# Performance work log

Hardware: AMD Instinct MI355X
Metric: run time of the kernel (lower is better)

## Reference

```python
import jax, jax.numpy as jnp
import numpy as np

NX = 96
N_NODES = 6 * NX * NX          # 55296 cubed-sphere grid points
N_EDGES = 4 * N_NODES          # ~4-neighbor connectivity
HID = 32
NUM_STEPS = 3


def setup_inputs() -> dict:
    key = jax.random.key(0)
    ks = jax.random.split(key, 12)
    s = 0.05
    inp = {
        "in_node_features": jax.random.normal(ks[0], (2, 6, NX, NX, 32), jnp.float32),
        "edge_relation": jax.random.normal(ks[1], (N_EDGES, 4), jnp.float32),
        "pw1": jax.random.normal(ks[2], (32, HID), jnp.float32) * s,
        "pb1": jnp.zeros((HID,), jnp.float32),
        "pw2": jax.random.normal(ks[3], (HID, HID), jnp.float32) * s,
        "pb2": jnp.zeros((HID,), jnp.float32),
        "ew1": jax.random.normal(ks[4], (4, 32), jnp.float32) * s,
        "eb1": jnp.zeros((32,), jnp.float32),
        "ew2": jax.random.normal(ks[5], (32, HID * HID), jnp.float32) * s,
        "eb2": jnp.zeros((HID * HID,), jnp.float32),
        "conv_b": jnp.zeros((HID,), jnp.float32),
        "gru_w_ih": jax.random.normal(ks[6], (3 * HID, HID), jnp.float32) * s,
        "gru_w_hh": jax.random.normal(ks[7], (3 * HID, HID), jnp.float32) * s,
        "gru_b_ih": jnp.zeros((3 * HID,), jnp.float32),
        "gru_b_hh": jnp.zeros((3 * HID,), jnp.float32),
        "edge_src": jax.random.randint(ks[8], (N_EDGES,), 0, N_NODES, jnp.int32),
        "edge_dst": jax.random.randint(ks[9], (N_EDGES,), 0, N_NODES, jnp.int32),
    }
    return inp


def reference(in_node_features, edge_relation, pw1, pb1, pw2, pb2,
              ew1, eb1, ew2, eb2, conv_b,
              gru_w_ih, gru_w_hh, gru_b_ih, gru_b_hh,
              edge_src, edge_dst):
    B, T, nx1, nx2, C = in_node_features.shape
    N = T * nx1 * nx2
    H = pw2.shape[1]

    x = in_node_features.reshape(B, N, C)
    # project_node_features: Linear -> ReLU -> Linear
    h0 = jnp.maximum(x @ pw1 + pb1, 0.0) @ pw2 + pb2          # [B, N, H]

    # edge network (same every step): Linear -> ReLU -> Linear -> [E, H, H]
    We = (jnp.maximum(edge_relation @ ew1 + eb1, 0.0) @ ew2 + eb2)
    We = We.reshape(-1, H, H)                                  # [E, H, H]

    def seg_sum(m):  # m: [E, H] -> [N, H]
        return jax.ops.segment_sum(m, edge_dst, num_segments=N)

    def step(carry, _):
        node, hidden = carry                                   # each [B, N, H]
        # NNConv: gather src feats, per-edge matmul, scatter-sum to dst
        msg = jnp.einsum('beh,eho->beo', node[:, edge_src], We)  # [B, E, H]
        agg = jax.vmap(seg_sum)(msg) + conv_b                    # [B, N, H]
        node = jnp.maximum(agg, 0.0)                             # ReLU
        # single GRU step (seq_len = 1)
        gx = node @ gru_w_ih.T + gru_b_ih                        # [B, N, 3H]
        gh = hidden @ gru_w_hh.T + gru_b_hh
        r = jax.nn.sigmoid(gx[..., :H] + gh[..., :H])
        z = jax.nn.sigmoid(gx[..., H:2 * H] + gh[..., H:2 * H])
        n = jnp.tanh(gx[..., 2 * H:] + r * gh[..., 2 * H:])
        hidden = (1.0 - z) * n + z * hidden
        return (hidden, hidden), None

    (node, _), _ = jax.lax.scan(step, (h0, h0), None, length=NUM_STEPS)
    return node.reshape(B, T, nx1, nx2, H)
```

## Files before the change

kernel.cpp:

```cpp
#include <hip/hip_runtime.h>

typedef unsigned short u16;
typedef short s16x8 __attribute__((ext_vector_type(8)));
typedef float f32x4 __attribute__((ext_vector_type(4)));
typedef float f32x2 __attribute__((ext_vector_type(2)));

#define NNODES 55296
#define NEDGES 221184
#define ROWS   110592

__device__ __forceinline__ u16 f2bf(float f) {
    union { float f; unsigned u; } v; v.f = f;
    unsigned r = (v.u + 0x7fffu + ((v.u >> 16) & 1u)) >> 16;
    return (u16)r;
}
__device__ __forceinline__ float bf2f(u16 u) {
    return __uint_as_float(((unsigned)u) << 16);
}

__global__ __launch_bounds__(256) void pack_bfrag(
    const float* __restrict__ src, u16* __restrict__ dst_hi, u16* __restrict__ dst_lo,
    int ntiles, int ncols, int trans)
{
    int idx = blockIdx.x * 256 + threadIdx.x;
    if (idx >= ntiles * 512) return;
    int t = idx >> 9, rr = idx & 511, lane = rr >> 3, j = rr & 7;
    int k = (lane >> 4) * 8 + j;
    int n = t * 16 + (lane & 15);
    float v = trans ? src[n * 32 + k] : src[k * ncols + n];
    u16 hb = f2bf(v);
    dst_hi[idx] = hb;
    if (dst_lo) dst_lo[idx] = f2bf(v - bf2f(hb));
}

__global__ __launch_bounds__(256) void edgemlp_kernel(
    const float* __restrict__ er, const float* __restrict__ ew1,
    const float* __restrict__ eb1, u16* __restrict__ rbf)
{
    __shared__ float er_lds[32];
    __shared__ float w_lds[128];
    __shared__ float b_lds[32];
    int tid = threadIdx.x;
    int e8 = blockIdx.x * 8;
    if (tid < 32) er_lds[tid] = er[e8 * 4 + tid];
    else if (tid < 160) w_lds[tid - 32] = ew1[tid - 32];
    else if (tid < 192) b_lds[tid - 160] = eb1[tid - 160];
    __syncthreads();
    int el = tid >> 5, o = tid & 31;
    const float* e4 = er_lds + el * 4;
    float v = b_lds[o] + e4[0] * w_lds[o] + e4[1] * w_lds[32 + o]
                       + e4[2] * w_lds[64 + o] + e4[3] * w_lds[96 + o];
    rbf[(e8 + el) * 32 + o] = f2bf(fmaxf(v, 0.f));
}

__global__ __launch_bounds__(256) void nodeproj_kernel(
    const float* __restrict__ x,
    const u16* __restrict__ pw1h, const u16* __restrict__ pw1l, const float* __restrict__ pb1,
    const u16* __restrict__ pw2h, const u16* __restrict__ pw2l, const float* __restrict__ pb2,
    float* __restrict__ st_f32, u16* __restrict__ st_hi, u16* __restrict__ st_lo)
{
    __shared__ alignas(16) u16 t_hi[4][512];
    __shared__ alignas(16) u16 t_lo[4][512];
    int tid = threadIdx.x, wave = tid >> 6, lane = tid & 63;
    int quad = lane >> 4, col = lane & 15;
    int row0 = (blockIdx.x * 4 + wave) * 16;

    const float* xp = x + (row0 + col) * 32 + quad * 8;
    f32x4 xv0 = *(const f32x4*)(xp), xv1 = *(const f32x4*)(xp + 4);
    s16x8 ah, al;
#pragma unroll
    for (int i = 0; i < 4; ++i) {
        u16 h0 = f2bf(xv0[i]); ah[i] = (short)h0; al[i] = (short)f2bf(xv0[i] - bf2f(h0));
        u16 h1 = f2bf(xv1[i]); ah[4+i] = (short)h1; al[4+i] = (short)f2bf(xv1[i] - bf2f(h1));
    }
#pragma unroll
    for (int t = 0; t < 2; ++t) {
        s16x8 bh = *(const s16x8*)(pw1h + t * 512 + lane * 8);
        s16x8 bl = *(const s16x8*)(pw1l + t * 512 + lane * 8);
        f32x4 acc = {0,0,0,0};
        acc = __builtin_amdgcn_mfma_f32_16x16x32_bf16(al, bh, acc, 0,0,0);
        acc = __builtin_amdgcn_mfma_f32_16x16x32_bf16(ah, bl, acc, 0,0,0);
        acc = __builtin_amdgcn_mfma_f32_16x16x32_bf16(ah, bh, acc, 0,0,0);
        float bias = pb1[t * 16 + col];
#pragma unroll
        for (int r = 0; r < 4; ++r) {
            float v = fmaxf(acc[r] + bias, 0.f);
            u16 hb = f2bf(v);
            int idx = (quad * 4 + r) * 32 + t * 16 + col;
            t_hi[wave][idx] = hb;
            t_lo[wave][idx] = f2bf(v - bf2f(hb));
        }
    }
    __syncthreads();
    s16x8 th = *(const s16x8*)(&t_hi[wave][col * 32 + quad * 8]);
    s16x8 tl = *(const s16x8*)(&t_lo[wave][col * 32 + quad * 8]);
#pragma unroll
    for (int t = 0; t < 2; ++t) {
        s16x8 bh = *(const s16x8*)(pw2h + t * 512 + lane * 8);
        s16x8 bl = *(const s16x8*)(pw2l + t * 512 + lane * 8);
        f32x4 acc = {0,0,0,0};
        acc = __builtin_amdgcn_mfma_f32_16x16x32_bf16(tl, bh, acc, 0,0,0);
        acc = __builtin_amdgcn_mfma_f32_16x16x32_bf16(th, bl, acc, 0,0,0);
        acc = __builtin_amdgcn_mfma_f32_16x16x32_bf16(th, bh, acc, 0,0,0);
        float bias = pb2[t * 16 + col];
#pragma unroll
        for (int r = 0; r < 4; ++r) {
            float v = acc[r] + bias;
            int row = row0 + quad * 4 + r;
            int o = t * 16 + col;
            st_f32[row * 32 + o] = v;
            u16 hb = f2bf(v);
            st_hi[row * 32 + o] = hb;
            st_lo[row * 32 + o] = f2bf(v - bf2f(hb));
        }
    }
}

__global__ __launch_bounds__(256) void msg_kernel(
    const u16* __restrict__ rbf, const u16* __restrict__ ew2f,
    const float* __restrict__ eb2, const float* __restrict__ state,
    const int* __restrict__ esrc, const int* __restrict__ edst,
    float* __restrict__ agg)
{
    __shared__ alignas(16) float eb2_lds[1024];
    __shared__ alignas(16) float ns_lds[4][16 * 68];
    int tid = threadIdx.x;
    {
        *(f32x4*)(eb2_lds + tid * 4) = *(const f32x4*)(eb2 + tid * 4);
    }
    int wave = tid >> 6, lane = tid & 63;
    int quad = lane >> 4, col = lane & 15;
    int e0 = (blockIdx.x * 4 + wave) * 16;

    s16x8 afrag = *(const s16x8*)(rbf + (e0 + col) * 32 + quad * 8);

    {
        int el = lane >> 2, part = lane & 3;
        int b = part >> 1, half = part & 1;
        int src = esrc[e0 + el];
        const float* sp = state + (b * NNODES + src) * 32 + half * 16;
        float* dp = &ns_lds[wave][el * 68 + b * 32 + half * 16];
        *(f32x4*)(dp + 0)  = *(const f32x4*)(sp + 0);
        *(f32x4*)(dp + 4)  = *(const f32x4*)(sp + 4);
        *(f32x4*)(dp + 8)  = *(const f32x4*)(sp + 8);
        *(f32x4*)(dp + 12) = *(const f32x4*)(sp + 12);
    }
    int dstid[4];
#pragma unroll
    for (int r = 0; r < 4; ++r) dstid[r] = edst[e0 + quad * 4 + r];
    __syncthreads();

    float msg[2][2][4] = {};
    const float* nsw = &ns_lds[wave][0];
#pragma unroll 4
    for (int hh = 0; hh < 16; ++hh) {
        int h0 = hh * 2, h1 = hh * 2 + 1;
        s16x8 b0 = *(const s16x8*)(ew2f + (4 * hh + 0) * 512 + lane * 8);
        s16x8 b1 = *(const s16x8*)(ew2f + (4 * hh + 1) * 512 + lane * 8);
        s16x8 b2 = *(const s16x8*)(ew2f + (4 * hh + 2) * 512 + lane * 8);
        s16x8 b3 = *(const s16x8*)(ew2f + (4 * hh + 3) * 512 + lane * 8);
        f32x4 z = {0,0,0,0};
        f32x4 d0 = __builtin_amdgcn_mfma_f32_16x16x32_bf16(afrag, b0, z, 0,0,0);
        f32x4 d1 = __builtin_amdgcn_mfma_f32_16x16x32_bf16(afrag, b1, z, 0,0,0);
        f32x4 d2 = __builtin_amdgcn_mfma_f32_16x16x32_bf16(afrag, b2, z, 0,0,0);
        f32x4 d3 = __builtin_amdgcn_mfma_f32_16x16x32_bf16(afrag, b3, z, 0,0,0);
        float e00 = eb2_lds[h0 * 32 + col],      e01 = eb2_lds[h0 * 32 + 16 + col];
        float e10 = eb2_lds[h1 * 32 + col],      e11 = eb2_lds[h1 * 32 + 16 + col];
#pragma unroll
        for (int r = 0; r < 4; ++r) {
            int e = quad * 4 + r;
            f32x2 n0 = *(const f32x2*)(nsw + e * 68 + 0 * 32 + h0);
            f32x2 n1 = *(const f32x2*)(nsw + e * 68 + 1 * 32 + h0);
            float w00 = d0[r] + e00, w01 = d1[r] + e01;
            float w10 = d2[r] + e10, w11 = d3[r] + e11;
            msg[0][0][r] += n0.x * w00 + n0.y * w10;
            msg[0][1][r] += n0.x * w01 + n0.y * w11;
            msg[1][0][r] += n1.x * w00 + n1.y * w10;
            msg[1][1][r] += n1.x * w01 + n1.y * w11;
        }
    }
#pragma unroll
    for (int r = 0; r < 4; ++r) {
#pragma unroll
        for (int b = 0; b < 2; ++b) {
            float* base = agg + (b * NNODES + dstid[r]) * 32;
            unsafeAtomicAdd(base + col,      msg[b][0][r]);
            unsafeAtomicAdd(base + 16 + col, msg[b][1][r]);
        }
    }
}

__global__ __launch_bounds__(256) void gru_kernel(
    const float* __restrict__ agg, const float* __restrict__ conv_b,
    const float* __restrict__ st_f32, const u16* __restrict__ st_hi, const u16* __restrict__ st_lo,
    const u16* __restrict__ wihh, const u16* __restrict__ wihl,
    const u16* __restrict__ whhh, const u16* __restrict__ whhl,
    const float* __restrict__ b_ih, const float* __restrict__ b_hh,
    float* __restrict__ out_f32, u16* __restrict__ out_hi, u16* __restrict__ out_lo)
{
    int tid = threadIdx.x, wave = tid >> 6, lane = tid & 63;
    int quad = lane >> 4, col = lane & 15;
    int row0 = (blockIdx.x * 4 + wave) * 16;

    const float* ap = agg + (row0 + col) * 32 + quad * 8;
    f32x4 av0 = *(const f32x4*)(ap), av1 = *(const f32x4*)(ap + 4);
    const float* cb = conv_b + quad * 8;
    f32x4 cb0 = *(const f32x4*)(cb), cb1 = *(const f32x4*)(cb + 4);
    s16x8 anh, anl;
#pragma unroll
    for (int i = 0; i < 4; ++i) {
        float v0 = fmaxf(av0[i] + cb0[i], 0.f);
        float v1 = fmaxf(av1[i] + cb1[i], 0.f);
        u16 h0 = f2bf(v0); anh[i] = (short)h0;   anl[i] = (short)f2bf(v0 - bf2f(h0));
        u16 h1 = f2bf(v1); anh[4+i] = (short)h1; anl[4+i] = (short)f2bf(v1 - bf2f(h1));
    }
    s16x8 ahh = *(const s16x8*)(st_hi + (row0 + col) * 32 + quad * 8);
    s16x8 ahl = *(const s16x8*)(st_lo + (row0 + col) * 32 + quad * 8);

    f32x4 gx[6], gh[6];
#pragma unroll
    for (int t = 0; t < 6; ++t) {
        s16x8 bh = *(const s16x8*)(wihh + t * 512 + lane * 8);
        s16x8 bl = *(const s16x8*)(wihl + t * 512 + lane * 8);
        f32x4 acc = {0,0,0,0};
        acc = __builtin_amdgcn_mfma_f32_16x16x32_bf16(anl, bh, acc, 0,0,0);
        acc = __builtin_amdgcn_mfma_f32_16x16x32_bf16(anh, bl, acc, 0,0,0);
        acc = __builtin_amdgcn_mfma_f32_16x16x32_bf16(anh, bh, acc, 0,0,0);
        gx[t] = acc;
        s16x8 ch = *(const s16x8*)(whhh + t * 512 + lane * 8);
        s16x8 cl = *(const s16x8*)(whhl + t * 512 + lane * 8);
        f32x4 acc2 = {0,0,0,0};
        acc2 = __builtin_amdgcn_mfma_f32_16x16x32_bf16(ahl, ch, acc2, 0,0,0);
        acc2 = __builtin_amdgcn_mfma_f32_16x16x32_bf16(ahh, cl, acc2, 0,0,0);
        acc2 = __builtin_amdgcn_mfma_f32_16x16x32_bf16(ahh, ch, acc2, 0,0,0);
        gh[t] = acc2;
    }
    float bihv[6], bhhv[6];
#pragma unroll
    for (int t = 0; t < 6; ++t) { bihv[t] = b_ih[t * 16 + col]; bhhv[t] = b_hh[t * 16 + col]; }

#pragma unroll
    for (int r = 0; r < 4; ++r) {
        int row = row0 + quad * 4 + r;
#pragma unroll
        for (int oh = 0; oh < 2; ++oh) {
            int o = oh * 16 + col;
            float hid = st_f32[row * 32 + o];
            float sr = (gx[oh][r] + bihv[oh]) + (gh[oh][r] + bhhv[oh]);
            float sz = (gx[2+oh][r] + bihv[2+oh]) + (gh[2+oh][r] + bhhv[2+oh]);
            float gxn = gx[4+oh][r] + bihv[4+oh];
            float ghn = gh[4+oh][r] + bhhv[4+oh];
            float rr = 1.f / (1.f + __expf(-sr));
            float zz = 1.f / (1.f + __expf(-sz));
            float narg = gxn + rr * ghn;
            float ex = __expf(2.f * narg);
            float nn = (ex - 1.f) / (ex + 1.f);
            float hnew = (1.f - zz) * nn + zz * hid;
            out_f32[row * 32 + o] = hnew;
            u16 hb = f2bf(hnew);
            out_hi[row * 32 + o] = hb;
            out_lo[row * 32 + o] = f2bf(hnew - bf2f(hb));
        }
    }
}

extern "C" void kernel_launch(void* const* d_in, const int* in_sizes, int n_in,
                              void* d_out, int out_size, void* d_ws, size_t ws_size,
                              hipStream_t stream)
{
    const float* x      = (const float*)d_in[0];
    const float* er     = (const float*)d_in[1];
    const float* pw1    = (const float*)d_in[2];
    const float* pb1    = (const float*)d_in[3];
    const float* pw2    = (const float*)d_in[4];
    const float* pb2    = (const float*)d_in[5];
    const float* ew1    = (const float*)d_in[6];
    const float* eb1    = (const float*)d_in[7];
    const float* ew2    = (const float*)d_in[8];
    const float* eb2    = (const float*)d_in[9];
    const float* conv_b = (const float*)d_in[10];
    const float* wih    = (const float*)d_in[11];
    const float* whh    = (const float*)d_in[12];
    const float* bih    = (const float*)d_in[13];
    const float* bhh    = (const float*)d_in[14];
    const int*   esrc   = (const int*)d_in[15];
    const int*   edst   = (const int*)d_in[16];
    float* out = (float*)d_out;

    char* ws = (char*)d_ws;
    size_t off = 0;
    auto alloc = [&](size_t bytes) -> void* {
        void* p = ws + off;
        off = (off + bytes + 255) & ~(size_t)255;
        return p;
    };
    u16*   rbf    = (u16*)  alloc((size_t)NEDGES * 32 * 2);
    float* st_f32 = (float*)alloc((size_t)ROWS * 32 * 4);
    u16*   st_hi  = (u16*)  alloc((size_t)ROWS * 32 * 2);
    u16*   st_lo  = (u16*)  alloc((size_t)ROWS * 32 * 2);
    float* agg    = (float*)alloc((size_t)ROWS * 32 * 4);
    u16*   ew2f   = (u16*)  alloc(64 * 512 * 2);
    u16*   pw1h   = (u16*)  alloc(2 * 512 * 2);
    u16*   pw1l   = (u16*)  alloc(2 * 512 * 2);
    u16*   pw2h   = (u16*)  alloc(2 * 512 * 2);
    u16*   pw2l   = (u16*)  alloc(2 * 512 * 2);
    u16*   wihhf  = (u16*)  alloc(6 * 512 * 2);
    u16*   wihlf  = (u16*)  alloc(6 * 512 * 2);
    u16*   whhhf  = (u16*)  alloc(6 * 512 * 2);
    u16*   whhlf  = (u16*)  alloc(6 * 512 * 2);
    (void)in_sizes; (void)n_in; (void)out_size; (void)ws_size;

    pack_bfrag<<<128, 256, 0, stream>>>(ew2, ew2f, (u16*)nullptr, 64, 1024, 0);
    pack_bfrag<<<4,   256, 0, stream>>>(pw1, pw1h, pw1l, 2, 32, 0);
    pack_bfrag<<<4,   256, 0, stream>>>(pw2, pw2h, pw2l, 2, 32, 0);
    pack_bfrag<<<12,  256, 0, stream>>>(wih, wihhf, wihlf, 6, 96, 1);
    pack_bfrag<<<12,  256, 0, stream>>>(whh, whhhf, whhlf, 6, 96, 1);

    edgemlp_kernel<<<NEDGES / 8, 256, 0, stream>>>(er, ew1, eb1, rbf);
    nodeproj_kernel<<<ROWS / 64, 256, 0, stream>>>(x, pw1h, pw1l, pb1, pw2h, pw2l, pb2,
                                                   st_f32, st_hi, st_lo);
    for (int s = 0; s < 3; ++s) {
        hipMemsetAsync(agg, 0, (size_t)ROWS * 32 * 4, stream);
        msg_kernel<<<NEDGES / 64, 256, 0, stream>>>(rbf, ew2f, eb2, st_f32, esrc, edst, agg);
        float* of = (s == 2) ? out : st_f32;
        gru_kernel<<<ROWS / 64, 256, 0, stream>>>(agg, conv_b, st_f32, st_hi, st_lo,
                                                  wihhf, wihlf, whhhf, whhlf, bih, bhh,
                                                  of, st_hi, st_lo);
    }
}
```

Before: 385.3 us.

## Sort edges by destination, merge pack kernels, fuse agg zeroing, widen msg/gru tiles

```diff
diff --git a/kernel.cpp b/kernel.cpp
--- a/kernel.cpp
+++ b/kernel.cpp
@@ -8,6 +8,7 @@
 #define NNODES 55296
 #define NEDGES 221184
 #define ROWS   110592
+#define MFMA   __builtin_amdgcn_mfma_f32_16x16x32_bf16
 
 __device__ __forceinline__ u16 f2bf(float f) {
     union { float f; unsigned u; } v; v.f = f;
@@ -18,46 +19,109 @@
     return __uint_as_float(((unsigned)u) << 16);
 }
 
-__global__ __launch_bounds__(256) void pack_bfrag(
-    const float* __restrict__ src, u16* __restrict__ dst_hi, u16* __restrict__ dst_lo,
-    int ntiles, int ncols, int trans)
-{
-    int idx = blockIdx.x * 256 + threadIdx.x;
-    if (idx >= ntiles * 512) return;
+__global__ __launch_bounds__(256) void hist_kernel(
+    const int* __restrict__ edst, int* __restrict__ cnt)
+{
+    int e = blockIdx.x * 256 + threadIdx.x;
+    atomicAdd(&cnt[edst[e]], 1);
+}
+
+__global__ __launch_bounds__(256) void scan1_kernel(
+    const int* __restrict__ cnt, int* __restrict__ base, int* __restrict__ csum)
+{
+    __shared__ int s[256];
+    int tid = threadIdx.x, gid = blockIdx.x * 256 + tid;
+    int v = cnt[gid]; s[tid] = v;
+    for (int off = 1; off < 256; off <<= 1) {
+        __syncthreads();
+        int t = (tid >= off) ? s[tid - off] : 0;
+        __syncthreads();
+        s[tid] += t;
+    }
+    __syncthreads();
+    base[gid] = s[tid] - v;
+    if (tid == 255) csum[blockIdx.x] = s[255];
+}
+
+__global__ __launch_bounds__(256) void scan2_kernel(int* __restrict__ csum)
+{
+    __shared__ int s[256];
+    int tid = threadIdx.x;
+    int v = (tid < 216) ? csum[tid] : 0;
+    s[tid] = v;
+    for (int off = 1; off < 256; off <<= 1) {
+        __syncthreads();
+        int t = (tid >= off) ? s[tid - off] : 0;
+        __syncthreads();
+        s[tid] += t;
+    }
+    __syncthreads();
+    if (tid < 216) csum[tid] = s[tid] - v;
+}
+
+__global__ __launch_bounds__(256) void scatter_kernel(
+    const int* __restrict__ edst, const int* __restrict__ esrc,
+    int* __restrict__ base, const int* __restrict__ csum,
+    int* __restrict__ perm, int* __restrict__ srcS, int* __restrict__ dstS)
+{
+    int e = blockIdx.x * 256 + threadIdx.x;
+    int v = edst[e];
+    int idx = csum[v >> 8] + atomicAdd(&base[v], 1);
+    perm[idx] = e;
+    srcS[idx] = esrc[e];
+    dstS[idx] = v;
+}
+
+__global__ __launch_bounds__(256) void pack_all(
+    const float* __restrict__ ew2, const float* __restrict__ pw1,
+    const float* __restrict__ pw2, const float* __restrict__ wih,
+    const float* __restrict__ whh,
+    u16* __restrict__ ew2h, u16* __restrict__ ew2l,
+    u16* __restrict__ pw1h, u16* __restrict__ pw1l,
+    u16* __restrict__ pw2h, u16* __restrict__ pw2l,
+    u16* __restrict__ wihh, u16* __restrict__ wihl,
+    u16* __restrict__ whhh, u16* __restrict__ whhl)
+{
+    int b = blockIdx.x;
+    const float* src; u16 *dh, *dl; int ncols, trans, lb;
+    if      (b < 128) { src = ew2; dh = ew2h; dl = ew2l; ncols = 1024; trans = 0; lb = b; }
+    else if (b < 132) { src = pw1; dh = pw1h; dl = pw1l; ncols = 32;   trans = 0; lb = b - 128; }
+    else if (b < 136) { src = pw2; dh = pw2h; dl = pw2l; ncols = 32;   trans = 0; lb = b - 132; }
+    else if (b < 148) { src = wih; dh = wihh; dl = wihl; ncols = 32;   trans = 1; lb = b - 136; }
+    else              { src = whh; dh = whhh; dl = whhl; ncols = 32;   trans = 1; lb = b - 148; }
+    int idx = lb * 256 + threadIdx.x;
     int t = idx >> 9, rr = idx & 511, lane = rr >> 3, j = rr & 7;
     int k = (lane >> 4) * 8 + j;
     int n = t * 16 + (lane & 15);
     float v = trans ? src[n * 32 + k] : src[k * ncols + n];
     u16 hb = f2bf(v);
-    dst_hi[idx] = hb;
-    if (dst_lo) dst_lo[idx] = f2bf(v - bf2f(hb));
+    dh[idx] = hb;
+    dl[idx] = f2bf(v - bf2f(hb));
 }
 
 __global__ __launch_bounds__(256) void edgemlp_kernel(
     const float* __restrict__ er, const float* __restrict__ ew1,
-    const float* __restrict__ eb1, u16* __restrict__ rbf)
-{
-    __shared__ float er_lds[32];
-    __shared__ float w_lds[128];
-    __shared__ float b_lds[32];
-    int tid = threadIdx.x;
-    int e8 = blockIdx.x * 8;
-    if (tid < 32) er_lds[tid] = er[e8 * 4 + tid];
-    else if (tid < 160) w_lds[tid - 32] = ew1[tid - 32];
-    else if (tid < 192) b_lds[tid - 160] = eb1[tid - 160];
-    __syncthreads();
-    int el = tid >> 5, o = tid & 31;
-    const float* e4 = er_lds + el * 4;
-    float v = b_lds[o] + e4[0] * w_lds[o] + e4[1] * w_lds[32 + o]
-                       + e4[2] * w_lds[64 + o] + e4[3] * w_lds[96 + o];
-    rbf[(e8 + el) * 32 + o] = f2bf(fmaxf(v, 0.f));
+    const float* __restrict__ eb1, const int* __restrict__ perm,
+    u16* __restrict__ rbf, u16* __restrict__ rbfl)
+{
+    int gid = blockIdx.x * 256 + threadIdx.x;
+    int e = gid >> 5, o = gid & 31;
+    int pe = perm[e];
+    f32x4 e4 = *(const f32x4*)(er + (size_t)pe * 4);
+    float v = eb1[o] + e4[0] * ew1[o] + e4[1] * ew1[32 + o]
+                     + e4[2] * ew1[64 + o] + e4[3] * ew1[96 + o];
+    float vr = fmaxf(v, 0.f);
+    u16 hb = f2bf(vr);
+    rbf[gid]  = hb;
+    rbfl[gid] = f2bf(vr - bf2f(hb));
 }
 
 __global__ __launch_bounds__(256) void nodeproj_kernel(
     const float* __restrict__ x,
     const u16* __restrict__ pw1h, const u16* __restrict__ pw1l, const float* __restrict__ pb1,
     const u16* __restrict__ pw2h, const u16* __restrict__ pw2l, const float* __restrict__ pb2,
-    float* __restrict__ st_f32, u16* __restrict__ st_hi, u16* __restrict__ st_lo)
+    float* __restrict__ st_f32, u16* __restrict__ st_hi, u16* __restrict__ st_lo,
+    float* __restrict__ agg)
 {
     __shared__ alignas(16) u16 t_hi[4][512];
     __shared__ alignas(16) u16 t_lo[4][512];
@@ -65,7 +129,14 @@
     int quad = lane >> 4, col = lane & 15;
     int row0 = (blockIdx.x * 4 + wave) * 16;
 
-    const float* xp = x + (row0 + col) * 32 + quad * 8;
+    {
+        float* az = agg + (size_t)blockIdx.x * 64 * 32;
+        f32x4 zz = {0.f, 0.f, 0.f, 0.f};
+        *(f32x4*)(az + tid * 8)     = zz;
+        *(f32x4*)(az + tid * 8 + 4) = zz;
+    }
+
+    const float* xp = x + (size_t)(row0 + col) * 32 + quad * 8;
     f32x4 xv0 = *(const f32x4*)(xp), xv1 = *(const f32x4*)(xp + 4);
     s16x8 ah, al;
 #pragma unroll
@@ -78,9 +149,9 @@
         s16x8 bh = *(const s16x8*)(pw1h + t * 512 + lane * 8);
         s16x8 bl = *(const s16x8*)(pw1l + t * 512 + lane * 8);
         f32x4 acc = {0,0,0,0};
-        acc = __builtin_amdgcn_mfma_f32_16x16x32_bf16(al, bh, acc, 0,0,0);
-        acc = __builtin_amdgcn_mfma_f32_16x16x32_bf16(ah, bl, acc, 0,0,0);
-        acc = __builtin_amdgcn_mfma_f32_16x16x32_bf16(ah, bh, acc, 0,0,0);
+        acc = MFMA(al, bh, acc, 0,0,0);
+        acc = MFMA(ah, bl, acc, 0,0,0);
+        acc = MFMA(ah, bh, acc, 0,0,0);
         float bias = pb1[t * 16 + col];
 #pragma unroll
         for (int r = 0; r < 4; ++r) {
@@ -99,167 +170,218 @@
         s16x8 bh = *(const s16x8*)(pw2h + t * 512 + lane * 8);
         s16x8 bl = *(const s16x8*)(pw2l + t * 512 + lane * 8);
         f32x4 acc = {0,0,0,0};
-        acc = __builtin_amdgcn_mfma_f32_16x16x32_bf16(tl, bh, acc, 0,0,0);
-        acc = __builtin_amdgcn_mfma_f32_16x16x32_bf16(th, bl, acc, 0,0,0);
-        acc = __builtin_amdgcn_mfma_f32_16x16x32_bf16(th, bh, acc, 0,0,0);
+        acc = MFMA(tl, bh, acc, 0,0,0);
+        acc = MFMA(th, bl, acc, 0,0,0);
+        acc = MFMA(th, bh, acc, 0,0,0);
         float bias = pb2[t * 16 + col];
 #pragma unroll
         for (int r = 0; r < 4; ++r) {
             float v = acc[r] + bias;
             int row = row0 + quad * 4 + r;
             int o = t * 16 + col;
-            st_f32[row * 32 + o] = v;
+            st_f32[(size_t)row * 32 + o] = v;
             u16 hb = f2bf(v);
-            st_hi[row * 32 + o] = hb;
-            st_lo[row * 32 + o] = f2bf(v - bf2f(hb));
-        }
-    }
-}
-
-__global__ __launch_bounds__(256) void msg_kernel(
-    const u16* __restrict__ rbf, const u16* __restrict__ ew2f,
+            st_hi[(size_t)row * 32 + o] = hb;
+            st_lo[(size_t)row * 32 + o] = f2bf(v - bf2f(hb));
+        }
+    }
+}
+
+__global__ __launch_bounds__(256, 4) void msg_kernel(
+    const u16* __restrict__ rbf, const u16* __restrict__ rbfl,
+    const u16* __restrict__ ew2h, const u16* __restrict__ ew2l,
     const float* __restrict__ eb2, const float* __restrict__ state,
-    const int* __restrict__ esrc, const int* __restrict__ edst,
+    const int* __restrict__ srcS, const int* __restrict__ dstS,
     float* __restrict__ agg)
 {
     __shared__ alignas(16) float eb2_lds[1024];
-    __shared__ alignas(16) float ns_lds[4][16 * 68];
+    __shared__ alignas(16) float ns_lds[4][32 * 68];
     int tid = threadIdx.x;
-    {
-        *(f32x4*)(eb2_lds + tid * 4) = *(const f32x4*)(eb2 + tid * 4);
-    }
+    *(f32x4*)(eb2_lds + tid * 4) = *(const f32x4*)(eb2 + tid * 4);
+
     int wave = tid >> 6, lane = tid & 63;
     int quad = lane >> 4, col = lane & 15;
-    int e0 = (blockIdx.x * 4 + wave) * 16;
-
-    s16x8 afrag = *(const s16x8*)(rbf + (e0 + col) * 32 + quad * 8);
+    int e0 = (blockIdx.x * 4 + wave) * 32;
+
+    s16x8 afh0 = *(const s16x8*)(rbf  + (size_t)(e0 + col) * 32 + quad * 8);
+    s16x8 afh1 = *(const s16x8*)(rbf  + (size_t)(e0 + 16 + col) * 32 + quad * 8);
+    s16x8 afl0 = *(const s16x8*)(rbfl + (size_t)(e0 + col) * 32 + quad * 8);
+    s16x8 afl1 = *(const s16x8*)(rbfl + (size_t)(e0 + 16 + col) * 32 + quad * 8);
 
     {
-        int el = lane >> 2, part = lane & 3;
-        int b = part >> 1, half = part & 1;
-        int src = esrc[e0 + el];
-        const float* sp = state + (b * NNODES + src) * 32 + half * 16;
-        float* dp = &ns_lds[wave][el * 68 + b * 32 + half * 16];
-        *(f32x4*)(dp + 0)  = *(const f32x4*)(sp + 0);
-        *(f32x4*)(dp + 4)  = *(const f32x4*)(sp + 4);
-        *(f32x4*)(dp + 8)  = *(const f32x4*)(sp + 8);
-        *(f32x4*)(dp + 12) = *(const f32x4*)(sp + 12);
-    }
-    int dstid[4];
-#pragma unroll
-    for (int r = 0; r < 4; ++r) dstid[r] = edst[e0 + quad * 4 + r];
+        int el = lane >> 1, b = lane & 1;
+        int src = srcS[e0 + el];
+        const float* sp = state + ((size_t)b * NNODES + src) * 32;
+        float* dp = &ns_lds[wave][el * 68 + b * 32];
+#pragma unroll
+        for (int c = 0; c < 8; ++c) *(f32x4*)(dp + c * 4) = *(const f32x4*)(sp + c * 4);
+    }
+    int dstA[2][4];
+    {
+        int4 d0 = *(const int4*)(dstS + e0 + quad * 4);
+        int4 d1 = *(const int4*)(dstS + e0 + 16 + quad * 4);
+        dstA[0][0]=d0.x; dstA[0][1]=d0.y; dstA[0][2]=d0.z; dstA[0][3]=d0.w;
+        dstA[1][0]=d1.x; dstA[1][1]=d1.y; dstA[1][2]=d1.z; dstA[1][3]=d1.w;
+    }
     __syncthreads();
 
-    float msg[2][2][4] = {};
+    f32x2 mv[2][2][4];
+#pragma unroll
+    for (int f = 0; f < 2; ++f)
+#pragma unroll
+        for (int b = 0; b < 2; ++b)
+#pragma unroll
+            for (int r = 0; r < 4; ++r) { mv[f][b][r].x = 0.f; mv[f][b][r].y = 0.f; }
+
     const float* nsw = &ns_lds[wave][0];
-#pragma unroll 4
+#pragma unroll 2
     for (int hh = 0; hh < 16; ++hh) {
-        int h0 = hh * 2, h1 = hh * 2 + 1;
-        s16x8 b0 = *(const s16x8*)(ew2f + (4 * hh + 0) * 512 + lane * 8);
-        s16x8 b1 = *(const s16x8*)(ew2f + (4 * hh + 1) * 512 + lane * 8);
-        s16x8 b2 = *(const s16x8*)(ew2f + (4 * hh + 2) * 512 + lane * 8);
-        s16x8 b3 = *(const s16x8*)(ew2f + (4 * hh + 3) * 512 + lane * 8);
-        f32x4 z = {0,0,0,0};
-        f32x4 d0 = __builtin_amdgcn_mfma_f32_16x16x32_bf16(afrag, b0, z, 0,0,0);
-        f32x4 d1 = __builtin_amdgcn_mfma_f32_16x16x32_bf16(afrag, b1, z, 0,0,0);
-        f32x4 d2 = __builtin_amdgcn_mfma_f32_16x16x32_bf16(afrag, b2, z, 0,0,0);
-        f32x4 d3 = __builtin_amdgcn_mfma_f32_16x16x32_bf16(afrag, b3, z, 0,0,0);
-        float e00 = eb2_lds[h0 * 32 + col],      e01 = eb2_lds[h0 * 32 + 16 + col];
-        float e10 = eb2_lds[h1 * 32 + col],      e11 = eb2_lds[h1 * 32 + 16 + col];
-#pragma unroll
-        for (int r = 0; r < 4; ++r) {
-            int e = quad * 4 + r;
-            f32x2 n0 = *(const f32x2*)(nsw + e * 68 + 0 * 32 + h0);
-            f32x2 n1 = *(const f32x2*)(nsw + e * 68 + 1 * 32 + h0);
-            float w00 = d0[r] + e00, w01 = d1[r] + e01;
-            float w10 = d2[r] + e10, w11 = d3[r] + e11;
-            msg[0][0][r] += n0.x * w00 + n0.y * w10;
-            msg[0][1][r] += n0.x * w01 + n0.y * w11;
-            msg[1][0][r] += n1.x * w00 + n1.y * w10;
-            msg[1][1][r] += n1.x * w01 + n1.y * w11;
-        }
-    }
-#pragma unroll
-    for (int r = 0; r < 4; ++r) {
+        int h0 = hh * 2;
+        f32x4 d[2][4];
+#pragma unroll
+        for (int t = 0; t < 4; ++t) {
+            s16x8 bh = *(const s16x8*)(ew2h + (size_t)(4 * hh + t) * 512 + lane * 8);
+            s16x8 bl = *(const s16x8*)(ew2l + (size_t)(4 * hh + t) * 512 + lane * 8);
+            f32x4 z = {0,0,0,0};
+            f32x4 a0 = MFMA(afl0, bh, z, 0,0,0);
+            a0 = MFMA(afh0, bl, a0, 0,0,0);
+            a0 = MFMA(afh0, bh, a0, 0,0,0);
+            d[0][t] = a0;
+            f32x4 a1 = MFMA(afl1, bh, z, 0,0,0);
+            a1 = MFMA(afh1, bl, a1, 0,0,0);
+            a1 = MFMA(afh1, bh, a1, 0,0,0);
+            d[1][t] = a1;
+        }
+        f32x2 eb0 = { eb2_lds[h0 * 32 + col],      eb2_lds[h0 * 32 + 16 + col] };
+        f32x2 eb1v= { eb2_lds[h0 * 32 + 32 + col], eb2_lds[h0 * 32 + 48 + col] };
+#pragma unroll
+        for (int f = 0; f < 2; ++f) {
+#pragma unroll
+            for (int r = 0; r < 4; ++r) {
+                int e = f * 16 + quad * 4 + r;
+                f32x2 n0 = *(const f32x2*)(nsw + e * 68 + h0);
+                f32x2 n1 = *(const f32x2*)(nsw + e * 68 + 32 + h0);
+                f32x2 w0 = { d[f][0][r] + eb0.x,  d[f][1][r] + eb0.y };
+                f32x2 w1 = { d[f][2][r] + eb1v.x, d[f][3][r] + eb1v.y };
+                mv[f][0][r] += n0.x * w0 + n0.y * w1;
+                mv[f][1][r] += n1.x * w0 + n1.y * w1;
+            }
+        }
+    }
+
+#pragma unroll
+    for (int f = 0; f < 2; ++f) {
 #pragma unroll
         for (int b = 0; b < 2; ++b) {
-            float* base = agg + (b * NNODES + dstid[r]) * 32;
-            unsafeAtomicAdd(base + col,      msg[b][0][r]);
-            unsafeAtomicAdd(base + 16 + col, msg[b][1][r]);
+            f32x2 acc = {0.f, 0.f};
+#pragma unroll
+            for (int r = 0; r < 4; ++r) {
+                acc += mv[f][b][r];
+                bool flush = (r == 3) || (dstA[f][r + 1] != dstA[f][r]);
+                if (flush) {
+                    float* bp = agg + ((size_t)b * NNODES + dstA[f][r]) * 32;
+                    unsafeAtomicAdd(bp + col,      acc.x);
+                    unsafeAtomicAdd(bp + 16 + col, acc.y);
+                    acc.x = 0.f; acc.y = 0.f;
+                }
+            }
         }
     }
 }
 
 __global__ __launch_bounds__(256) void gru_kernel(
-    const float* __restrict__ agg, const float* __restrict__ conv_b,
-    const float* __restrict__ st_f32, const u16* __restrict__ st_hi, const u16* __restrict__ st_lo,
+    float* __restrict__ agg, const float* __restrict__ conv_b,
+    const float* st_f32, const u16* st_hi, const u16* st_lo,
     const u16* __restrict__ wihh, const u16* __restrict__ wihl,
     const u16* __restrict__ whhh, const u16* __restrict__ whhl,
     const float* __restrict__ b_ih, const float* __restrict__ b_hh,
-    float* __restrict__ out_f32, u16* __restrict__ out_hi, u16* __restrict__ out_lo)
+    float* out_f32, u16* out_hi, u16* out_lo)
 {
     int tid = threadIdx.x, wave = tid >> 6, lane = tid & 63;
     int quad = lane >> 4, col = lane & 15;
-    int row0 = (blockIdx.x * 4 + wave) * 16;
-
-    const float* ap = agg + (row0 + col) * 32 + quad * 8;
-    f32x4 av0 = *(const f32x4*)(ap), av1 = *(const f32x4*)(ap + 4);
+    int row0 = (blockIdx.x * 4 + wave) * 32;
+
     const float* cb = conv_b + quad * 8;
-    f32x4 cb0 = *(const f32x4*)(cb), cb1 = *(const f32x4*)(cb + 4);
-    s16x8 anh, anl;
-#pragma unroll
-    for (int i = 0; i < 4; ++i) {
-        float v0 = fmaxf(av0[i] + cb0[i], 0.f);
-        float v1 = fmaxf(av1[i] + cb1[i], 0.f);
-        u16 h0 = f2bf(v0); anh[i] = (short)h0;   anl[i] = (short)f2bf(v0 - bf2f(h0));
-        u16 h1 = f2bf(v1); anh[4+i] = (short)h1; anl[4+i] = (short)f2bf(v1 - bf2f(h1));
-    }
-    s16x8 ahh = *(const s16x8*)(st_hi + (row0 + col) * 32 + quad * 8);
-    s16x8 ahl = *(const s16x8*)(st_lo + (row0 + col) * 32 + quad * 8);
-
-    f32x4 gx[6], gh[6];
+    f32x4 cb0 = *(const f32x4*)cb, cb1 = *(const f32x4*)(cb + 4);
+
+    s16x8 anh[2], anl[2], ahh[2], ahl[2];
+#pragma unroll
+    for (int f = 0; f < 2; ++f) {
+        size_t ro = (size_t)(row0 + f * 16 + col) * 32 + quad * 8;
+        float* ap = agg + ro;
+        f32x4 av0 = *(const f32x4*)ap, av1 = *(const f32x4*)(ap + 4);
+        f32x4 zz = {0.f,0.f,0.f,0.f};
+        *(f32x4*)ap = zz; *(f32x4*)(ap + 4) = zz;
+#pragma unroll
+        for (int i = 0; i < 4; ++i) {
+            float v0 = fmaxf(av0[i] + cb0[i], 0.f);
+            float v1 = fmaxf(av1[i] + cb1[i], 0.f);
+            u16 h0 = f2bf(v0); anh[f][i] = (short)h0;   anl[f][i] = (short)f2bf(v0 - bf2f(h0));
+            u16 h1 = f2bf(v1); anh[f][4+i] = (short)h1; anl[f][4+i] = (short)f2bf(v1 - bf2f(h1));
+        }
+        ahh[f] = *(const s16x8*)(st_hi + ro);
+        ahl[f] = *(const s16x8*)(st_lo + ro);
+    }
+
+    float hidv[2][4][2];
+#pragma unroll
+    for (int f = 0; f < 2; ++f)
+#pragma unroll
+        for (int r = 0; r < 4; ++r) {
+            int row = row0 + f * 16 + quad * 4 + r;
+            hidv[f][r][0] = st_f32[(size_t)row * 32 + col];
+            hidv[f][r][1] = st_f32[(size_t)row * 32 + 16 + col];
+        }
+
+    f32x4 gx[2][6], gh[2][6];
 #pragma unroll
     for (int t = 0; t < 6; ++t) {
         s16x8 bh = *(const s16x8*)(wihh + t * 512 + lane * 8);
         s16x8 bl = *(const s16x8*)(wihl + t * 512 + lane * 8);
-        f32x4 acc = {0,0,0,0};
-        acc = __builtin_amdgcn_mfma_f32_16x16x32_bf16(anl, bh, acc, 0,0,0);
-        acc = __builtin_amdgcn_mfma_f32_16x16x32_bf16(anh, bl, acc, 0,0,0);
-        acc = __builtin_amdgcn_mfma_f32_16x16x32_bf16(anh, bh, acc, 0,0,0);
-        gx[t] = acc;
         s16x8 ch = *(const s16x8*)(whhh + t * 512 + lane * 8);
         s16x8 cl = *(const s16x8*)(whhl + t * 512 + lane * 8);
-        f32x4 acc2 = {0,0,0,0};
-        acc2 = __builtin_amdgcn_mfma_f32_16x16x32_bf16(ahl, ch, acc2, 0,0,0);
-        acc2 = __builtin_amdgcn_mfma_f32_16x16x32_bf16(ahh, cl, acc2, 0,0,0);
-        acc2 = __builtin_amdgcn_mfma_f32_16x16x32_bf16(ahh, ch, acc2, 0,0,0);
-        gh[t] = acc2;
+#pragma unroll
+        for (int f = 0; f < 2; ++f) {
+            f32x4 a = {0,0,0,0};
+            a = MFMA(anl[f], bh, a, 0,0,0);
+            a = MFMA(anh[f], bl, a, 0,0,0);
+            a = MFMA(anh[f], bh, a, 0,0,0);
+            gx[f][t] = a;
+            f32x4 c = {0,0,0,0};
+            c = MFMA(ahl[f], ch, c, 0,0,0);
+            c = MFMA(ahh[f], cl, c, 0,0,0);
+            c = MFMA(ahh[f], ch, c, 0,0,0);
+            gh[f][t] = c;
+        }
     }
     float bihv[6], bhhv[6];
 #pragma unroll
     for (int t = 0; t < 6; ++t) { bihv[t] = b_ih[t * 16 + col]; bhhv[t] = b_hh[t * 16 + col]; }
 
 #pragma unroll
-    for (int r = 0; r < 4; ++r) {
-        int row = row0 + quad * 4 + r;
-#pragma unroll
-        for (int oh = 0; oh < 2; ++oh) {
-            int o = oh * 16 + col;
-            float hid = st_f32[row * 32 + o];
-            float sr = (gx[oh][r] + bihv[oh]) + (gh[oh][r] + bhhv[oh]);
-            float sz = (gx[2+oh][r] + bihv[2+oh]) + (gh[2+oh][r] + bhhv[2+oh]);
-            float gxn = gx[4+oh][r] + bihv[4+oh];
-            float ghn = gh[4+oh][r] + bhhv[4+oh];
-            float rr = 1.f / (1.f + __expf(-sr));
-            float zz = 1.f / (1.f + __expf(-sz));
-            float narg = gxn + rr * ghn;
-            float ex = __expf(2.f * narg);
-            float nn = (ex - 1.f) / (ex + 1.f);
-            float hnew = (1.f - zz) * nn + zz * hid;
-            out_f32[row * 32 + o] = hnew;
-            u16 hb = f2bf(hnew);
-            out_hi[row * 32 + o] = hb;
-            out_lo[row * 32 + o] = f2bf(hnew - bf2f(hb));
+    for (int f = 0; f < 2; ++f) {
+#pragma unroll
+        for (int r = 0; r < 4; ++r) {
+            int row = row0 + f * 16 + quad * 4 + r;
+#pragma unroll
+            for (int oh = 0; oh < 2; ++oh) {
+                int o = oh * 16 + col;
+                float hid = hidv[f][r][oh];
+                float sr = (gx[f][oh][r] + bihv[oh]) + (gh[f][oh][r] + bhhv[oh]);
+                float sz = (gx[f][2+oh][r] + bihv[2+oh]) + (gh[f][2+oh][r] + bhhv[2+oh]);
+                float gxn = gx[f][4+oh][r] + bihv[4+oh];
+                float ghn = gh[f][4+oh][r] + bhhv[4+oh];
+                float rr = 1.f / (1.f + __expf(-sr));
+                float zz = 1.f / (1.f + __expf(-sz));
+                float narg = gxn + rr * ghn;
+                float ex = __expf(2.f * narg);
+                float nn = (ex - 1.f) / (ex + 1.f);
+                float hnew = (1.f - zz) * nn + zz * hid;
+                out_f32[(size_t)row * 32 + o] = hnew;
+                u16 hb = f2bf(hnew);
+                out_hi[(size_t)row * 32 + o] = hb;
+                out_lo[(size_t)row * 32 + o] = f2bf(hnew - bf2f(hb));
+            }
         }
     }
 }
@@ -295,11 +417,13 @@
         return p;
     };
     u16*   rbf    = (u16*)  alloc((size_t)NEDGES * 32 * 2);
+    u16*   rbfl   = (u16*)  alloc((size_t)NEDGES * 32 * 2);
     float* st_f32 = (float*)alloc((size_t)ROWS * 32 * 4);
     u16*   st_hi  = (u16*)  alloc((size_t)ROWS * 32 * 2);
     u16*   st_lo  = (u16*)  alloc((size_t)ROWS * 32 * 2);
     float* agg    = (float*)alloc((size_t)ROWS * 32 * 4);
-    u16*   ew2f   = (u16*)  alloc(64 * 512 * 2);
+    u16*   ew2fh  = (u16*)  alloc(64 * 512 * 2);
+    u16*   ew2fl  = (u16*)  alloc(64 * 512 * 2);
     u16*   pw1h   = (u16*)  alloc(2 * 512 * 2);
     u16*   pw1l   = (u16*)  alloc(2 * 512 * 2);
     u16*   pw2h   = (u16*)  alloc(2 * 512 * 2);
@@ -308,23 +432,33 @@
     u16*   wihlf  = (u16*)  alloc(6 * 512 * 2);
     u16*   whhhf  = (u16*)  alloc(6 * 512 * 2);
     u16*   whhlf  = (u16*)  alloc(6 * 512 * 2);
+    int*   cnt    = (int*)  alloc((size_t)NNODES * 4);
+    int*   base   = (int*)  alloc((size_t)NNODES * 4);
+    int*   csum   = (int*)  alloc(256 * 4);
+    int*   perm   = (int*)  alloc((size_t)NEDGES * 4);
+    int*   srcS   = (int*)  alloc((size_t)NEDGES * 4);
+    int*   dstS   = (int*)  alloc((size_t)NEDGES * 4);
     (void)in_sizes; (void)n_in; (void)out_size; (void)ws_size;
 
-    pack_bfrag<<<128, 256, 0, stream>>>(ew2, ew2f, (u16*)nullptr, 64, 1024, 0);
-    pack_bfrag<<<4,   256, 0, stream>>>(pw1, pw1h, pw1l, 2, 32, 0);
-    pack_bfrag<<<4,   256, 0, stream>>>(pw2, pw2h, pw2l, 2, 32, 0);
-    pack_bfrag<<<12,  256, 0, stream>>>(wih, wihhf, wihlf, 6, 96, 1);
-    pack_bfrag<<<12,  256, 0, stream>>>(whh, whhhf, whhlf, 6, 96, 1);
-
-    edgemlp_kernel<<<NEDGES / 8, 256, 0, stream>>>(er, ew1, eb1, rbf);
+    hipMemsetAsync(cnt, 0, (size_t)NNODES * 4, stream);
+    hist_kernel   <<<NEDGES / 256, 256, 0, stream>>>(edst, cnt);
+    scan1_kernel  <<<NNODES / 256, 256, 0, stream>>>(cnt, base, csum);
+    scan2_kernel  <<<1,            256, 0, stream>>>(csum);
+    scatter_kernel<<<NEDGES / 256, 256, 0, stream>>>(edst, esrc, base, csum, perm, srcS, dstS);
+
+    pack_all<<<160, 256, 0, stream>>>(ew2, pw1, pw2, wih, whh,
+                                      ew2fh, ew2fl, pw1h, pw1l, pw2h, pw2l,
+                                      wihhf, wihlf, whhhf, whhlf);
+    edgemlp_kernel<<<NEDGES * 32 / 256, 256, 0, stream>>>(er, ew1, eb1, perm, rbf, rbfl);
     nodeproj_kernel<<<ROWS / 64, 256, 0, stream>>>(x, pw1h, pw1l, pb1, pw2h, pw2l, pb2,
-                                                   st_f32, st_hi, st_lo);
+                                                   st_f32, st_hi, st_lo, agg);
+
     for (int s = 0; s < 3; ++s) {
-        hipMemsetAsync(agg, 0, (size_t)ROWS * 32 * 4, stream);
-        msg_kernel<<<NEDGES / 64, 256, 0, stream>>>(rbf, ew2f, eb2, st_f32, esrc, edst, agg);
+        msg_kernel<<<NEDGES / 128, 256, 0, stream>>>(rbf, rbfl, ew2fh, ew2fl, eb2,
+                                                     st_f32, srcS, dstS, agg);
         float* of = (s == 2) ? out : st_f32;
-        gru_kernel<<<ROWS / 64, 256, 0, stream>>>(agg, conv_b, st_f32, st_hi, st_lo,
-                                                  wihhf, wihlf, whhhf, whhlf, bih, bhh,
-                                                  of, st_hi, st_lo);
-    }
-}
+        gru_kernel<<<ROWS / 128, 256, 0, stream>>>(agg, conv_b, st_f32, st_hi, st_lo,
+                                                   wihhf, wihlf, whhhf, whhlf, bih, bhh,
+                                                   of, st_hi, st_lo);
+    }
+}
```

Result: slower. 515.2 us (+33.7%).
